# Performance work log

Hardware: AMD Instinct MI355X
Metric: run time of the kernel (lower is better)

The kernel has to match this reference:

```python
import jax, jax.numpy as jnp
import numpy as np

B, N, C = 4, 65536, 192
HEADS = 6
HEADC = C // HEADS
EPS = 1e-5


def _ln(x, w, b):
    # custom LayerNorm: unbiased std (ddof=1), divide by (std + eps)
    m = x.mean(-1, keepdims=True)
    s = jnp.std(x, axis=-1, keepdims=True, ddof=1)
    return w * ((x - m) / (s + EPS)) + b


def setup_inputs() -> dict:
    key = jax.random.key(0)
    ks = jax.random.split(key, 8)
    x = jax.random.normal(ks[0], (B, N, C), dtype=jnp.float32)
    # 1x1 conv weights == channel matmuls; [out_c, in_c]
    qkv_w = jax.random.normal(ks[1], (3 * C, C), dtype=jnp.float32) * 0.05
    qkv_b = jax.random.normal(ks[2], (3 * C,), dtype=jnp.float32) * 0.02
    o1_w = jax.random.normal(ks[3], (C, C), dtype=jnp.float32) * 0.05
    o1_b = jax.random.normal(ks[4], (C,), dtype=jnp.float32) * 0.02
    o2_w = jax.random.normal(ks[5], (C, C), dtype=jnp.float32) * 0.05
    o2_b = jax.random.normal(ks[6], (C,), dtype=jnp.float32) * 0.02
    kln_w = jnp.ones((HEADS, 1, HEADC), dtype=jnp.float32)
    kln_b = jnp.zeros((HEADS, 1, HEADC), dtype=jnp.float32)
    vln_w = jnp.ones((HEADS, 1, HEADC), dtype=jnp.float32)
    vln_b = jnp.zeros((HEADS, 1, HEADC), dtype=jnp.float32)
    return {"x": x, "qkv_w": qkv_w, "qkv_b": qkv_b, "o1_w": o1_w,
            "o1_b": o1_b, "o2_w": o2_w, "o2_b": o2_b,
            "kln_w": kln_w, "kln_b": kln_b, "vln_w": vln_w, "vln_b": vln_b,
            "H": 256, "W": 256}


def reference(x, qkv_w, qkv_b, o1_w, o1_b, o2_w, o2_b,
              kln_w, kln_b, vln_w, vln_b, H, W):
    b, n, c = x.shape
    heads, headc = kln_w.shape[0], kln_w.shape[-1]
    # 1x1 conv QKV projection (per-pixel linear)
    qkv = jnp.einsum('bnc,dc->bnd', x, qkv_w) + qkv_b          # [B,N,3C]
    qkv = qkv.reshape(b, n, heads, 3 * headc).transpose(0, 2, 1, 3)  # [B,h,N,3d]
    q, k, v = jnp.split(qkv, 3, axis=-1)                        # each [B,h,N,d]
    k = _ln(k, kln_w, kln_b)
    v = _ln(v, vln_w, vln_b)
    # Galerkin (softmax-free) linear attention
    kv = jnp.einsum('bhnd,bhne->bhde', k, v) / n                # [B,h,d,d]
    attn = jnp.einsum('bhnd,bhde->bhne', q, kv)                 # [B,h,N,d]
    attn = attn.transpose(0, 2, 1, 3).reshape(b, n, c)          # [B,N,C]
    ret = attn + x                                              # residual
    h = jax.nn.gelu(jnp.einsum('bnc,dc->bnd', ret, o1_w) + o1_b,
                    approximate=False)
    out = jnp.einsum('bnc,dc->bnd', h, o2_w) + o2_b + x
    return out
```

## Files before the change

### kernel.cpp

```cpp
#include <hip/hip_runtime.h>
#include <math.h>

typedef __attribute__((ext_vector_type(8)))  __bf16 bf16x8;
typedef __attribute__((ext_vector_type(16))) float  f32x16;
typedef __attribute__((ext_vector_type(4)))  float  f32x4;
typedef __attribute__((ext_vector_type(4)))  int    i32x4;
typedef __attribute__((ext_vector_type(4)))  unsigned u32x4;

union FR { bf16x8 v; u32x4 q; unsigned u[4]; };

__device__ inline f32x16 MF(bf16x8 a, bf16x8 b, f32x16 c) {
    return __builtin_amdgcn_mfma_f32_32x32x16_bf16(a, b, c, 0, 0, 0);
}
__device__ inline unsigned pk(float a, float b) {
    unsigned ua = (__builtin_bit_cast(unsigned, a) + 0x8000u) >> 16;
    unsigned ub = (__builtin_bit_cast(unsigned, b) + 0x8000u) >> 16;
    return ua | (ub << 16);
}
__device__ inline unsigned short bfr(float a) {
    return (unsigned short)((__builtin_bit_cast(unsigned, a) + 0x8000u) >> 16);
}
__device__ inline float ubf(unsigned short s) {
    return __builtin_bit_cast(float, (unsigned)s << 16);
}
__device__ inline float gelu_f(float g) {
    float z  = g * 0.70710678118654752f;
    float az = fabsf(z);
    float t  = 1.0f / (1.0f + 0.3275911f * az);
    float poly = t*(0.254829592f + t*(-0.284496736f + t*(1.421413741f +
                 t*(-1.453152027f + t*1.061405429f))));
    float er = 1.0f - poly * __expf(-az * az);
    er = (z < 0.f) ? -er : er;
    return 0.5f * g * (1.0f + er);
}

__global__ void k0_pack(const float* __restrict__ qkv_w, const float* __restrict__ qkv_b,
                        const float* __restrict__ o2w,
                        unsigned* __restrict__ wkvpk, unsigned* __restrict__ o2pk,
                        float* __restrict__ bkv)
{
    int idx = blockIdx.x * 256 + threadIdx.x;
    if (idx < 36864) {
        int kt = idx / 3072, r = idx % 3072, nt = r / 256, r3 = r % 256;
        int l = r3 >> 2, q = r3 & 3;
        int c  = kt * 16 + (l >> 5) * 8 + q * 2;
        int rp = nt * 32 + (l & 31);
        int row = (rp >> 6) * 96 + 32 + (rp & 63);
        wkvpk[idx] = pk(qkv_w[row * 192 + c], qkv_w[row * 192 + c + 1]);
    } else if (idx < 55296) {
        int i2 = idx - 36864;
        int kt = i2 / 1536, r = i2 % 1536, jt = r / 256, r3 = r % 256;
        int l = r3 >> 2, q = r3 & 3;
        int jj = kt * 16 + (l >> 5) * 8 + q * 2;
        int j  = jt * 32 + (l & 31);
        o2pk[i2] = pk(o2w[j * 192 + jj], o2w[j * 192 + jj + 1]);
    } else if (idx < 55680) {
        int rp = idx - 55296;
        bkv[rp] = qkv_b[(rp >> 6) * 96 + 32 + (rp & 63)];
    }
}

__global__ __launch_bounds__(256, 2)
void k1(const float* __restrict__ x, const u32x4* __restrict__ Wpk,
        const float* __restrict__ bkv, float* __restrict__ part)
{
    __shared__ __align__(16) float s1[6][16][64];
    __shared__ float skv[12][64];
    __shared__ __align__(16) float scr[4][64 * 34];
    __shared__ __align__(8)  float st[4][2][32][2];

    const int tid = threadIdx.x;
    const int wid = tid >> 6, lane = tid & 63;
    const int col = lane & 31, lh = lane >> 5;
    const int g = blockIdx.x, b = g >> 7, gb = g & 127;

    for (int i = tid; i < 6144; i += 256) ((float*)s1)[i] = 0.f;
    for (int i = tid; i < 768;  i += 256) ((float*)skv)[i] = 0.f;
    __syncthreads();

    float* sc  = scr[wid];
    float* stw = (float*)st[wid];

    for (int it = 0; it < 4; ++it) {
        const int sp = gb * 16 + wid * 4 + it;
        const float* xr = x + ((long)(b * 65536 + sp * 32 + col)) * 192 + lh * 8;
        FR afr[12];
#pragma unroll
        for (int kt = 0; kt < 12; ++kt) {
            f32x4 a0 = *(const f32x4*)(xr + kt * 16);
            f32x4 a1 = *(const f32x4*)(xr + kt * 16 + 4);
            afr[kt].u[0] = pk(a0.x, a0.y); afr[kt].u[1] = pk(a0.z, a0.w);
            afr[kt].u[2] = pk(a1.x, a1.y); afr[kt].u[3] = pk(a1.z, a1.w);
        }

        for (int h = 0; h < 6; ++h) {
            f32x16 acck = (f32x16)(bkv[(2 * h) * 32 + col]);
            f32x16 accv = (f32x16)(bkv[(2 * h + 1) * 32 + col]);
#pragma unroll
            for (int kt = 0; kt < 12; ++kt) {
                FR bk_, bv_;
                bk_.q = Wpk[(kt * 12 + 2 * h) * 64 + lane];
                bv_.q = Wpk[(kt * 12 + 2 * h + 1) * 64 + lane];
                acck = MF(afr[kt].v, bk_.v, acck);
                accv = MF(afr[kt].v, bv_.v, accv);
            }
#pragma unroll
            for (int r = 0; r < 16; r += 2) {
                int p = (r & 3) + 4 * lh + 8 * (r >> 2);
                *(float2*)&sc[col * 34 + p]        = make_float2(acck[r], acck[r + 1]);
                *(float2*)&sc[(32 + col) * 34 + p] = make_float2(accv[r], accv[r + 1]);
            }
            __builtin_amdgcn_wave_barrier();
            {
                const float* cb = sc + (lh * 32) * 34 + col;
                float s = 0.f, s2 = 0.f;
#pragma unroll
                for (int ch = 0; ch < 32; ++ch) {
                    float v = cb[ch * 34];
                    s += v; s2 = fmaf(v, v, s2);
                }
                float m   = s * (1.f / 32.f);
                float var = fmaxf((s2 - 32.f * m * m) * (1.f / 31.f), 0.f);
                float inv = 1.f / (sqrtf(var) + 1e-5f);
                *(float2*)&stw[(lh * 32 + col) * 2] = make_float2(m, inv);
            }
            __builtin_amdgcn_wave_barrier();
            float skl = 0.f, svl = 0.f;
            unsigned pkk[8], pkv[8];
#pragma unroll
            for (int j = 0; j < 8; ++j) {
                int r0 = 2 * j;
                int p0 = (r0 & 3) + 4 * lh + 8 * (r0 >> 2);
                float2 a0 = *(float2*)&stw[p0 * 2];
                float2 a1 = *(float2*)&stw[(p0 + 1) * 2];
                float2 c0 = *(float2*)&stw[(32 + p0) * 2];
                float2 c1 = *(float2*)&stw[(32 + p0 + 1) * 2];
                float k0 = (acck[r0]     - a0.x) * a0.y;
                float k1v = (acck[r0 + 1] - a1.x) * a1.y;
                float v0 = (accv[r0]     - c0.x) * c0.y;
                float v1 = (accv[r0 + 1] - c1.x) * c1.y;
                skl += k0 + k1v; svl += v0 + v1;
                pkk[j] = pk(k0, k1v); pkv[j] = pk(v0, v1);
            }
            atomicAdd(&skv[h][lane], skl);
            atomicAdd(&skv[6 + h][lane], svl);
            unsigned ka0 = __shfl_xor((int)(lh ? pkk[0] : pkk[2]), 32);
            unsigned ka1 = __shfl_xor((int)(lh ? pkk[1] : pkk[3]), 32);
            unsigned ka2 = __shfl_xor((int)(lh ? pkk[4] : pkk[6]), 32);
            unsigned ka3 = __shfl_xor((int)(lh ? pkk[5] : pkk[7]), 32);
            unsigned vb0 = __shfl_xor((int)(lh ? pkv[0] : pkv[2]), 32);
            unsigned vb1 = __shfl_xor((int)(lh ? pkv[1] : pkv[3]), 32);
            unsigned vb2 = __shfl_xor((int)(lh ? pkv[4] : pkv[6]), 32);
            unsigned vb3 = __shfl_xor((int)(lh ? pkv[5] : pkv[7]), 32);
            FR A0, A1, B0, B1;
            A0.u[0] = lh ? ka0 : pkk[0]; A0.u[1] = lh ? ka1 : pkk[1];
            A0.u[2] = lh ? pkk[2] : ka0; A0.u[3] = lh ? pkk[3] : ka1;
            A1.u[0] = lh ? ka2 : pkk[4]; A1.u[1] = lh ? ka3 : pkk[5];
            A1.u[2] = lh ? pkk[6] : ka2; A1.u[3] = lh ? pkk[7] : ka3;
            B0.u[0] = lh ? vb0 : pkv[0]; B0.u[1] = lh ? vb1 : pkv[1];
            B0.u[2] = lh ? pkv[2] : vb0; B0.u[3] = lh ? pkv[3] : vb1;
            B1.u[0] = lh ? vb2 : pkv[4]; B1.u[1] = lh ? vb3 : pkv[5];
            B1.u[2] = lh ? pkv[6] : vb2; B1.u[3] = lh ? pkv[7] : vb3;
            f32x16 ph = (f32x16)(0.f);
            ph = MF(A0.v, B0.v, ph);
            ph = MF(A1.v, B1.v, ph);
#pragma unroll
            for (int r = 0; r < 16; ++r) atomicAdd(&s1[h][r][lane], ph[r]);
            __builtin_amdgcn_wave_barrier();
        }
    }
    __syncthreads();
    float* pb = part + (long)g * 6912;
    for (int i = tid; i < 6144; i += 256) pb[i] = ((float*)s1)[i];
    for (int i = tid; i < 768;  i += 256) pb[6144 + i] = ((float*)skv)[i];
}

__global__ __launch_bounds__(1024)
void k1c(const float* __restrict__ part,
         const float* __restrict__ klnw, const float* __restrict__ klnb,
         const float* __restrict__ vlnw, const float* __restrict__ vlnb,
         float* __restrict__ kvg)
{
    __shared__ float sks[32], svs[32];
    const int bh = blockIdx.x, b = bh / 6, h = bh % 6;
    const int t = threadIdx.x;
    const int d = t >> 5, e = t & 31;
    const int lhd = (d >> 2) & 1, r = (d & 3) + 4 * (d >> 3);
    const float* pb = part + (long)(b * 128) * 6912;
    const int off = h * 1024 + r * 64 + (e + 32 * lhd);
    float s = 0.f;
#pragma unroll 4
    for (int w = 0; w < 128; ++w) s += pb[(long)w * 6912 + off];
    if (t < 64) {
        int tt = t & 31;
        int o2 = 6144 + (t < 32 ? 0 : 384) + h * 64 + tt;
        float acc = 0.f;
#pragma unroll 4
        for (int w = 0; w < 128; ++w)
            acc += pb[(long)w * 6912 + o2] + pb[(long)w * 6912 + o2 + 32];
        if (t < 32) sks[tt] = acc; else svs[tt] = acc;
    }
    __syncthreads();
    float kw = klnw[h * 32 + d], kb = klnb[h * 32 + d];
    float vw = vlnw[h * 32 + e], vb = vlnb[h * 32 + e];
    float kv = (kw * vw * s + kw * vb * sks[d] + kb * vw * svs[e]) * (1.f / 65536.f)
             + kb * vb;
    kvg[((b * 6 + h) * 32 + d) * 32 + e] = kv;
}

__global__ void k2a(const float* __restrict__ qkv_w, const float* __restrict__ qkv_b,
                    const float* __restrict__ kvg,
                    float* __restrict__ Pt, float* __restrict__ c0)
{
    int b = blockIdx.y;
    const float* kvb = kvg + (long)b * 6144;
    if (blockIdx.x < 144) {
        int idx = blockIdx.x * 256 + threadIdx.x;
        int c = idx % 192, cp = idx / 192;
        int h = cp >> 5, e = cp & 31;
        float s = 0.f;
#pragma unroll 8
        for (int d = 0; d < 32; ++d)
            s += qkv_w[(h * 96 + d) * 192 + c] * kvb[(h * 32 + d) * 32 + e];
        Pt[(long)b * 36864 + cp * 192 + c] = s;
    } else if (threadIdx.x < 192) {
        int cp = threadIdx.x, h = cp >> 5, e = cp & 31;
        float s = 0.f;
#pragma unroll 8
        for (int d = 0; d < 32; ++d)
            s += qkv_b[h * 96 + d] * kvb[(h * 32 + d) * 32 + e];
        c0[b * 192 + cp] = s;
    }
}

__global__ void k2b(const float* __restrict__ o1w, const float* __restrict__ o1b,
                    const float* __restrict__ Pt, const float* __restrict__ c0,
                    float* __restrict__ M1t, float* __restrict__ d1)
{
    int b = blockIdx.y;
    if (blockIdx.x < 144) {
        int idx = blockIdx.x * 256 + threadIdx.x;
        int c = idx % 192, j = idx / 192;
        float s = o1w[j * 192 + c];
        const float* pb = Pt + (long)b * 36864;
        const float* wr = o1w + j * 192;
#pragma unroll 8
        for (int cp = 0; cp < 192; ++cp)
            s += pb[cp * 192 + c] * wr[cp];
        M1t[(long)b * 36864 + j * 192 + c] = s;
    } else if (threadIdx.x < 192) {
        int j = threadIdx.x;
        float s = o1b[j];
        const float* wr = o1w + j * 192;
#pragma unroll 8
        for (int cp = 0; cp < 192; ++cp)
            s += c0[b * 192 + cp] * wr[cp];
        d1[b * 192 + j] = s;
    }
}

__global__ void k2c(const float* __restrict__ M1t, unsigned* __restrict__ M1pk)
{
    int idx = blockIdx.x * 256 + threadIdx.x;
    if (idx < 73728) {
        int b = idx / 18432, r = idx % 18432;
        int kt = r / 1536, r2 = r % 1536, jt = r2 / 256, r3 = r2 % 256;
        int l = r3 >> 2, q = r3 & 3;
        int c = kt * 16 + (l >> 5) * 8 + q * 2;
        int j = jt * 32 + (l & 31);
        const float* src = M1t + (long)b * 36864 + j * 192 + c;
        M1pk[idx] = pk(src[0], src[1]);
    }
}

__global__ __launch_bounds__(256, 2)
void k3(const float* __restrict__ x, const u32x4* __restrict__ M1bf,
        const float* __restrict__ d1, const u32x4* __restrict__ o2bf,
        const float* __restrict__ o2b, float* __restrict__ out)
{
    __shared__ __align__(16) unsigned short hbuf[4][32 * 200];
    const int tid = threadIdx.x;
    const int wid = tid >> 6, lane = tid & 63;
    const int col = lane & 31, lh = lane >> 5;
    const int w = blockIdx.x * 4 + wid;
    const int b = w >> 11, sp = w & 2047;

    const float* xrow = x + ((long)(b * 65536 + sp * 32)) * 192;
    const float* xr = xrow + col * 192 + lh * 8;
    FR afr[12];
#pragma unroll
    for (int kt = 0; kt < 12; ++kt) {
        f32x4 a0 = *(const f32x4*)(xr + kt * 16);
        f32x4 a1 = *(const f32x4*)(xr + kt * 16 + 4);
        afr[kt].u[0] = pk(a0.x, a0.y); afr[kt].u[1] = pk(a0.z, a0.w);
        afr[kt].u[2] = pk(a1.x, a1.y); afr[kt].u[3] = pk(a1.z, a1.w);
    }
    float d1v[6], o2bv[6];
#pragma unroll
    for (int jt = 0; jt < 6; ++jt) {
        d1v[jt]  = d1[b * 192 + jt * 32 + col];
        o2bv[jt] = o2b[jt * 32 + col];
    }

    f32x16 acc[6];
#pragma unroll
    for (int jt = 0; jt < 6; ++jt) acc[jt] = (f32x16)(d1v[jt]);
    const u32x4* W1 = M1bf + b * 4608;
#pragma unroll
    for (int kt = 0; kt < 12; ++kt) {
        bf16x8 av = afr[kt].v;
#pragma unroll
        for (int jt = 0; jt < 6; ++jt) {
            FR bv; bv.q = W1[(kt * 6 + jt) * 64 + lane];
            acc[jt] = MF(av, bv.v, acc[jt]);
        }
    }
    unsigned short* hb = hbuf[wid];
#pragma unroll
    for (int jt = 0; jt < 6; ++jt)
#pragma unroll
        for (int r = 0; r < 16; ++r) {
            int p = (r & 3) + 4 * lh + 8 * (r >> 2);
            hb[p * 200 + jt * 32 + col] = bfr(gelu_f(acc[jt][r]));
        }
    __syncthreads();
    i32x4 hfr[12];
#pragma unroll
    for (int kt = 0; kt < 12; ++kt)
        hfr[kt] = *(const i32x4*)&hb[col * 200 + kt * 16 + lh * 8];
    f32x16 acc2[6];
#pragma unroll
    for (int jt = 0; jt < 6; ++jt) acc2[jt] = (f32x16)(0.0f);
#pragma unroll
    for (int kt = 0; kt < 12; ++kt) {
        bf16x8 av = __builtin_bit_cast(bf16x8, hfr[kt]);
#pragma unroll
        for (int jt = 0; jt < 6; ++jt) {
            FR bv; bv.q = o2bf[(kt * 6 + jt) * 64 + lane];
            acc2[jt] = MF(av, bv.v, acc2[jt]);
        }
    }
    float* orow = out + ((long)(b * 65536 + sp * 32)) * 192;
#pragma unroll
    for (int jt = 0; jt < 6; ++jt) {
        int j = jt * 32 + col;
#pragma unroll
        for (int r = 0; r < 16; ++r) {
            int p = (r & 3) + 4 * lh + 8 * (r >> 2);
            orow[p * 192 + j] = acc2[jt][r] + o2bv[jt] + xrow[p * 192 + j];
        }
    }
}

extern "C" void kernel_launch(void* const* d_in, const int* in_sizes, int n_in,
                              void* d_out, int out_size, void* d_ws, size_t ws_size,
                              hipStream_t stream) {
    const float* x     = (const float*)d_in[0];
    const float* qkv_w = (const float*)d_in[1];
    const float* qkv_b = (const float*)d_in[2];
    const float* o1_w  = (const float*)d_in[3];
    const float* o1_b  = (const float*)d_in[4];
    const float* o2_w  = (const float*)d_in[5];
    const float* o2_b  = (const float*)d_in[6];
    const float* klnw  = (const float*)d_in[7];
    const float* klnb  = (const float*)d_in[8];
    const float* vlnw  = (const float*)d_in[9];
    const float* vlnb  = (const float*)d_in[10];
    float* out = (float*)d_out;
    float* ws  = (float*)d_ws;

    if (ws_size < (size_t)450432 * sizeof(float)) return;

    unsigned* wkvpk = (unsigned*)(ws);
    float*    bkv   = ws + 36864;
    float*    kvg   = ws + 37248;
    float*    Pt    = ws + 61824;
    float*    c0    = ws + 209280;
    float*    M1t   = ws + 210048;
    float*    d1    = ws + 357504;
    unsigned* M1pk  = (unsigned*)(ws + 358272);
    unsigned* o2pk  = (unsigned*)(ws + 432000);

    k0_pack<<<218, 256, 0, stream>>>(qkv_w, qkv_b, o2_w, wkvpk, o2pk, bkv);
    k1<<<512, 256, 0, stream>>>(x, (const u32x4*)wkvpk, bkv, (float*)d_out);
    k1c<<<24, 1024, 0, stream>>>((const float*)d_out, klnw, klnb, vlnw, vlnb, kvg);
    k2a<<<dim3(145, 4), 256, 0, stream>>>(qkv_w, qkv_b, kvg, Pt, c0);
    k2b<<<dim3(145, 4), 256, 0, stream>>>(o1_w, o1_b, Pt, c0, M1t, d1);
    k2c<<<288, 256, 0, stream>>>(M1t, M1pk);
    k3<<<2048, 256, 0, stream>>>(x, (const u32x4*)M1pk, d1, (const u32x4*)o2pk,
                                 o2_b, out);
}
```

Baseline: 764.6 us.

## Split k1 over head-pairs, stage weights in LDS, accumulate Gram in registers

The K/V statistics kernel k1 is restructured so each block handles one of three head-pairs, with its slice of packed K/V weights staged in LDS instead of re-read from global memory per head. The MFMA operand order is swapped so each lane's accumulator holds one pixel's channels, so the LayerNorm statistics come from in-register sums plus a cross-half shuffle. The Gram-matrix partials stay in registers rather than going through shared-memory atomics. Normalized K/V are transposed through a small bf16 LDS tile to form MFMA operands. The cost is that each x tile is now loaded three times (once per head-pair), and there are more partial buffers (512 per batch-head-pair) for k1c to reduce.

```diff
diff --git a/kernel.cpp b/kernel.cpp
--- a/kernel.cpp
+++ b/kernel.cpp
@@ -22,6 +22,18 @@
 }
 __device__ inline float ubf(unsigned short s) {
     return __builtin_bit_cast(float, (unsigned)s << 16);
+}
+__device__ inline float sum16(i32x4 a, i32x4 b) {
+    float s = 0.f;
+#pragma unroll
+    for (int i = 0; i < 4; ++i) {
+        unsigned ua = (unsigned)a[i], ub = (unsigned)b[i];
+        s += __builtin_bit_cast(float, ua << 16);
+        s += __builtin_bit_cast(float, ua & 0xffff0000u);
+        s += __builtin_bit_cast(float, ub << 16);
+        s += __builtin_bit_cast(float, ub & 0xffff0000u);
+    }
+    return s;
 }
 __device__ inline float gelu_f(float g) {
     float z  = g * 0.70710678118654752f;
@@ -64,25 +76,33 @@
 void k1(const float* __restrict__ x, const u32x4* __restrict__ Wpk,
         const float* __restrict__ bkv, float* __restrict__ part)
 {
-    __shared__ __align__(16) float s1[6][16][64];
-    __shared__ float skv[12][64];
-    __shared__ __align__(16) float scr[4][64 * 34];
-    __shared__ __align__(8)  float st[4][2][32][2];
+    __shared__ __align__(16) u32x4 Wlds[12][4][64];
+    __shared__ __align__(16) float biasl[2][2][2][16];
+    __shared__ __align__(16) unsigned short tr[4][32][40];
 
     const int tid = threadIdx.x;
     const int wid = tid >> 6, lane = tid & 63;
     const int col = lane & 31, lh = lane >> 5;
-    const int g = blockIdx.x, b = g >> 7, gb = g & 127;
-
-    for (int i = tid; i < 6144; i += 256) ((float*)s1)[i] = 0.f;
-    for (int i = tid; i < 768;  i += 256) ((float*)skv)[i] = 0.f;
+    const int bx = blockIdx.x, b = blockIdx.y;
+    const int chunk = bx / 3, hp = bx % 3;
+
+    for (int i = tid; i < 3072; i += 256) {
+        int kt = i >> 8, ntl = (i >> 6) & 3, l = i & 63;
+        Wlds[kt][ntl][l] = Wpk[(kt * 12 + hp * 4 + ntl) * 64 + l];
+    }
+    if (tid < 128) {
+        int hi = tid >> 6, kv = (tid >> 5) & 1, lhh = (tid >> 4) & 1, r = tid & 15;
+        int c = (r & 3) + 8 * (r >> 2) + 4 * lhh;
+        biasl[hi][kv][lhh][r] = bkv[(hp * 4 + hi * 2 + kv) * 32 + c];
+    }
     __syncthreads();
 
-    float* sc  = scr[wid];
-    float* stw = (float*)st[wid];
+    f32x16 gram[2] = { (f32x16)(0.f), (f32x16)(0.f) };
+    float ska[2] = {0.f, 0.f}, sva[2] = {0.f, 0.f};
+    unsigned short* tw = &tr[wid][0][0];
 
     for (int it = 0; it < 4; ++it) {
-        const int sp = gb * 16 + wid * 4 + it;
+        const int sp = chunk * 16 + wid * 4 + it;
         const float* xr = x + ((long)(b * 65536 + sp * 32 + col)) * 192 + lh * 8;
         FR afr[12];
 #pragma unroll
@@ -92,87 +112,88 @@
             afr[kt].u[0] = pk(a0.x, a0.y); afr[kt].u[1] = pk(a0.z, a0.w);
             afr[kt].u[2] = pk(a1.x, a1.y); afr[kt].u[3] = pk(a1.z, a1.w);
         }
-
-        for (int h = 0; h < 6; ++h) {
-            f32x16 acck = (f32x16)(bkv[(2 * h) * 32 + col]);
-            f32x16 accv = (f32x16)(bkv[(2 * h + 1) * 32 + col]);
+#pragma unroll
+        for (int hi = 0; hi < 2; ++hi) {
+            f32x16 acck = (f32x16)(0.f), accv = (f32x16)(0.f);
 #pragma unroll
             for (int kt = 0; kt < 12; ++kt) {
-                FR bk_, bv_;
-                bk_.q = Wpk[(kt * 12 + 2 * h) * 64 + lane];
-                bv_.q = Wpk[(kt * 12 + 2 * h + 1) * 64 + lane];
-                acck = MF(afr[kt].v, bk_.v, acck);
-                accv = MF(afr[kt].v, bv_.v, accv);
-            }
-#pragma unroll
-            for (int r = 0; r < 16; r += 2) {
-                int p = (r & 3) + 4 * lh + 8 * (r >> 2);
-                *(float2*)&sc[col * 34 + p]        = make_float2(acck[r], acck[r + 1]);
-                *(float2*)&sc[(32 + col) * 34 + p] = make_float2(accv[r], accv[r + 1]);
-            }
+                FR wk, wv;
+                wk.q = Wlds[kt][hi * 2][lane];
+                wv.q = Wlds[kt][hi * 2 + 1][lane];
+                acck = MF(wk.v, afr[kt].v, acck);
+                accv = MF(wv.v, afr[kt].v, accv);
+            }
+            f32x4 bk[4], bv[4];
+#pragma unroll
+            for (int q = 0; q < 4; ++q) {
+                bk[q] = *(const f32x4*)&biasl[hi][0][lh][q * 4];
+                bv[q] = *(const f32x4*)&biasl[hi][1][lh][q * 4];
+            }
+            float s = 0.f, s2 = 0.f;
+#pragma unroll
+            for (int r = 0; r < 16; ++r) {
+                acck[r] += bk[r >> 2][r & 3];
+                s += acck[r]; s2 = fmaf(acck[r], acck[r], s2);
+            }
+            s  += __shfl_xor(s, 32);
+            s2 += __shfl_xor(s2, 32);
+            float m   = s * (1.f / 32.f);
+            float var = fmaxf((s2 - 32.f * m * m) * (1.f / 31.f), 0.f);
+            float inv = 1.f / (sqrtf(var) + 1e-5f);
             __builtin_amdgcn_wave_barrier();
-            {
-                const float* cb = sc + (lh * 32) * 34 + col;
-                float s = 0.f, s2 = 0.f;
-#pragma unroll
-                for (int ch = 0; ch < 32; ++ch) {
-                    float v = cb[ch * 34];
-                    s += v; s2 = fmaf(v, v, s2);
-                }
-                float m   = s * (1.f / 32.f);
-                float var = fmaxf((s2 - 32.f * m * m) * (1.f / 31.f), 0.f);
-                float inv = 1.f / (sqrtf(var) + 1e-5f);
-                *(float2*)&stw[(lh * 32 + col) * 2] = make_float2(m, inv);
+#pragma unroll
+            for (int r = 0; r < 16; ++r) {
+                int c = (r & 3) + 8 * (r >> 2) + 4 * lh;
+                tw[c * 40 + col] = bfr((acck[r] - m) * inv);
             }
             __builtin_amdgcn_wave_barrier();
-            float skl = 0.f, svl = 0.f;
-            unsigned pkk[8], pkv[8];
-#pragma unroll
-            for (int j = 0; j < 8; ++j) {
-                int r0 = 2 * j;
-                int p0 = (r0 & 3) + 4 * lh + 8 * (r0 >> 2);
-                float2 a0 = *(float2*)&stw[p0 * 2];
-                float2 a1 = *(float2*)&stw[(p0 + 1) * 2];
-                float2 c0 = *(float2*)&stw[(32 + p0) * 2];
-                float2 c1 = *(float2*)&stw[(32 + p0 + 1) * 2];
-                float k0 = (acck[r0]     - a0.x) * a0.y;
-                float k1v = (acck[r0 + 1] - a1.x) * a1.y;
-                float v0 = (accv[r0]     - c0.x) * c0.y;
-                float v1 = (accv[r0 + 1] - c1.x) * c1.y;
-                skl += k0 + k1v; svl += v0 + v1;
-                pkk[j] = pk(k0, k1v); pkv[j] = pk(v0, v1);
-            }
-            atomicAdd(&skv[h][lane], skl);
-            atomicAdd(&skv[6 + h][lane], svl);
-            unsigned ka0 = __shfl_xor((int)(lh ? pkk[0] : pkk[2]), 32);
-            unsigned ka1 = __shfl_xor((int)(lh ? pkk[1] : pkk[3]), 32);
-            unsigned ka2 = __shfl_xor((int)(lh ? pkk[4] : pkk[6]), 32);
-            unsigned ka3 = __shfl_xor((int)(lh ? pkk[5] : pkk[7]), 32);
-            unsigned vb0 = __shfl_xor((int)(lh ? pkv[0] : pkv[2]), 32);
-            unsigned vb1 = __shfl_xor((int)(lh ? pkv[1] : pkv[3]), 32);
-            unsigned vb2 = __shfl_xor((int)(lh ? pkv[4] : pkv[6]), 32);
-            unsigned vb3 = __shfl_xor((int)(lh ? pkv[5] : pkv[7]), 32);
-            FR A0, A1, B0, B1;
-            A0.u[0] = lh ? ka0 : pkk[0]; A0.u[1] = lh ? ka1 : pkk[1];
-            A0.u[2] = lh ? pkk[2] : ka0; A0.u[3] = lh ? pkk[3] : ka1;
-            A1.u[0] = lh ? ka2 : pkk[4]; A1.u[1] = lh ? ka3 : pkk[5];
-            A1.u[2] = lh ? pkk[6] : ka2; A1.u[3] = lh ? pkk[7] : ka3;
-            B0.u[0] = lh ? vb0 : pkv[0]; B0.u[1] = lh ? vb1 : pkv[1];
-            B0.u[2] = lh ? pkv[2] : vb0; B0.u[3] = lh ? pkv[3] : vb1;
-            B1.u[0] = lh ? vb2 : pkv[4]; B1.u[1] = lh ? vb3 : pkv[5];
-            B1.u[2] = lh ? pkv[6] : vb2; B1.u[3] = lh ? pkv[7] : vb3;
-            f32x16 ph = (f32x16)(0.f);
-            ph = MF(A0.v, B0.v, ph);
-            ph = MF(A1.v, B1.v, ph);
-#pragma unroll
-            for (int r = 0; r < 16; ++r) atomicAdd(&s1[h][r][lane], ph[r]);
+            i32x4 kA0 = *(const i32x4*)&tw[col * 40 + lh * 8];
+            i32x4 kA1 = *(const i32x4*)&tw[col * 40 + 16 + lh * 8];
+            float rk = sum16(kA0, kA1);
+            rk += __shfl_xor(rk, 32);
+            ska[hi] += rk;
             __builtin_amdgcn_wave_barrier();
-        }
-    }
-    __syncthreads();
-    float* pb = part + (long)g * 6912;
-    for (int i = tid; i < 6144; i += 256) pb[i] = ((float*)s1)[i];
-    for (int i = tid; i < 768;  i += 256) pb[6144 + i] = ((float*)skv)[i];
+            s = 0.f; s2 = 0.f;
+#pragma unroll
+            for (int r = 0; r < 16; ++r) {
+                accv[r] += bv[r >> 2][r & 3];
+                s += accv[r]; s2 = fmaf(accv[r], accv[r], s2);
+            }
+            s  += __shfl_xor(s, 32);
+            s2 += __shfl_xor(s2, 32);
+            float m2   = s * (1.f / 32.f);
+            float var2 = fmaxf((s2 - 32.f * m2 * m2) * (1.f / 31.f), 0.f);
+            float inv2 = 1.f / (sqrtf(var2) + 1e-5f);
+#pragma unroll
+            for (int r = 0; r < 16; ++r) {
+                int c = (r & 3) + 8 * (r >> 2) + 4 * lh;
+                tw[c * 40 + col] = bfr((accv[r] - m2) * inv2);
+            }
+            __builtin_amdgcn_wave_barrier();
+            i32x4 vB0 = *(const i32x4*)&tw[col * 40 + lh * 8];
+            i32x4 vB1 = *(const i32x4*)&tw[col * 40 + 16 + lh * 8];
+            float rv = sum16(vB0, vB1);
+            rv += __shfl_xor(rv, 32);
+            sva[hi] += rv;
+            gram[hi] = MF(__builtin_bit_cast(bf16x8, kA0),
+                          __builtin_bit_cast(bf16x8, vB0), gram[hi]);
+            gram[hi] = MF(__builtin_bit_cast(bf16x8, kA1),
+                          __builtin_bit_cast(bf16x8, vB1), gram[hi]);
+            __builtin_amdgcn_wave_barrier();
+        }
+    }
+    const int widx = ((b * 3 + hp) * 128 + chunk) * 4 + wid;
+    float* pb = part + (long)widx * 2176;
+#pragma unroll
+    for (int hi = 0; hi < 2; ++hi) {
+#pragma unroll
+        for (int r = 0; r < 16; ++r)
+            pb[hi * 1024 + r * 64 + lane] = gram[hi][r];
+        if (lh == 0) {
+            pb[2048 + hi * 64 + col]      = ska[hi];
+            pb[2048 + hi * 64 + 32 + col] = sva[hi];
+        }
+    }
 }
 
 __global__ __launch_bounds__(1024)
@@ -183,21 +204,21 @@
 {
     __shared__ float sks[32], svs[32];
     const int bh = blockIdx.x, b = bh / 6, h = bh % 6;
+    const int hp = h >> 1, hi = h & 1;
     const int t = threadIdx.x;
     const int d = t >> 5, e = t & 31;
     const int lhd = (d >> 2) & 1, r = (d & 3) + 4 * (d >> 3);
-    const float* pb = part + (long)(b * 128) * 6912;
-    const int off = h * 1024 + r * 64 + (e + 32 * lhd);
+    const long p0 = (long)(b * 3 + hp) * 512;
+    const int off = hi * 1024 + r * 64 + (e + 32 * lhd);
     float s = 0.f;
 #pragma unroll 4
-    for (int w = 0; w < 128; ++w) s += pb[(long)w * 6912 + off];
+    for (int w = 0; w < 512; ++w) s += part[(p0 + w) * 2176 + off];
     if (t < 64) {
         int tt = t & 31;
-        int o2 = 6144 + (t < 32 ? 0 : 384) + h * 64 + tt;
+        int o2 = 2048 + hi * 64 + (t >> 5) * 32 + tt;
         float acc = 0.f;
 #pragma unroll 4
-        for (int w = 0; w < 128; ++w)
-            acc += pb[(long)w * 6912 + o2] + pb[(long)w * 6912 + o2 + 32];
+        for (int w = 0; w < 512; ++w) acc += part[(p0 + w) * 2176 + o2];
         if (t < 32) sks[tt] = acc; else svs[tt] = acc;
     }
     __syncthreads();
@@ -382,7 +403,7 @@
     unsigned* o2pk  = (unsigned*)(ws + 432000);
 
     k0_pack<<<218, 256, 0, stream>>>(qkv_w, qkv_b, o2_w, wkvpk, o2pk, bkv);
-    k1<<<512, 256, 0, stream>>>(x, (const u32x4*)wkvpk, bkv, (float*)d_out);
+    k1<<<dim3(384, 4), 256, 0, stream>>>(x, (const u32x4*)wkvpk, bkv, (float*)d_out);
     k1c<<<24, 1024, 0, stream>>>((const float*)d_out, klnw, klnb, vlnw, vlnb, kvg);
     k2a<<<dim3(145, 4), 256, 0, stream>>>(qkv_w, qkv_b, kvg, Pt, c0);
     k2b<<<dim3(145, 4), 256, 0, stream>>>(o1_w, o1_b, Pt, c0, M1t, d1);
```

Measured after the change: 646.9 us. 15.4% less time.
